# Optimization experiments

Measured on AMD Instinct MI355X. Metric: run time of the kernel, lower is better.

Reference implementation:

```python
import jax, jax.numpy as jnp
import numpy as np

D, N = 4, 2048  # d marginals, n bins


def setup_inputs() -> dict:
    key = jax.random.key(0)
    x = jax.random.uniform(key, (D, N), dtype=jnp.float32)
    return {"x": x}


def reference(x):
    # Greedy multi-marginal EMD (dEMD.forward with computeDual=False).
    # Sequential algorithm: at each step, look at the 'front' value of each of
    # the d rows (AA[i, idx[i]]), take the minimum mass, pay cost
    # (max(idx)-min(idx)) * minval, subtract it from every front, and advance
    # the pointer of the (first) argmin row. Loop ends when any pointer hits n.
    d, n = x.shape
    steps = d * (n - 1) + 1  # exact worst-case iteration count
    rows = jnp.arange(d)

    def step(carry, _):
        AA, idx, obj, done = carry
        vals = AA[rows, idx]                        # (d,) front values
        minval = jnp.min(vals)
        ind = jnp.argmin(vals)                      # first min, like vals.index(min)
        cost = (jnp.max(idx) - jnp.min(idx)).astype(AA.dtype)  # OBJ(idx)
        obj = obj + jnp.where(done, jnp.zeros((), AA.dtype), cost * minval)
        AA_new = AA.at[rows, idx].add(-minval)
        AA = jnp.where(done, AA, AA_new)
        idx_new = jnp.where(done, idx, idx.at[ind].add(1))
        done = done | jnp.any(idx_new >= n)
        return (AA, idx_new, obj, done), None

    init = (x,
            jnp.zeros(d, dtype=jnp.int32),
            jnp.zeros((), dtype=x.dtype),
            jnp.asarray(False))
    (_, _, obj, _), _ = jax.lax.scan(step, init, None, length=steps)
    return obj
```

## Files before the change

kernel.cpp:

```cpp
#include <hip/hip_runtime.h>


constexpr int D       = 4;
constexpr int N       = 2048;
constexpr int THREADS = 256;
constexpr int PER_LANE = N / 64;

__global__ __launch_bounds__(THREADS)
void demd_kernel(const float* __restrict__ x, float* __restrict__ out) {
    __shared__ float  S[D][N];
    __shared__ double red[THREADS];

    const int t    = threadIdx.x;
    const int wave = t >> 6;
    const int lane = t & 63;

    {
        const float* row = x + wave * N + lane * PER_LANE;
        float v[PER_LANE];
        #pragma unroll
        for (int k = 0; k < PER_LANE / 4; ++k) {
            float4 f = ((const float4*)row)[k];
            v[4*k+0] = f.x; v[4*k+1] = f.y; v[4*k+2] = f.z; v[4*k+3] = f.w;
        }
        double tot = 0.0;
        #pragma unroll
        for (int k = 0; k < PER_LANE; ++k) tot += (double)v[k];

        double scan = tot;
        #pragma unroll
        for (int off = 1; off < 64; off <<= 1) {
            double up = __shfl_up(scan, off, 64);
            if (lane >= off) scan += up;
        }
        double run = scan - tot;
        float* Srow = &S[wave][lane * PER_LANE];
        #pragma unroll
        for (int k = 0; k < PER_LANE; ++k) {
            run += (double)v[k];
            Srow[k] = (float)run;
        }
    }
    __syncthreads();

    float tend = S[0][N - 1];
    #pragma unroll
    for (int r = 1; r < D; ++r) tend = fminf(tend, S[r][N - 1]);

    double acc = 0.0;
    #pragma unroll
    for (int k = 0; k < N / THREADS; ++k) {
        const int j = t + k * THREADS;
        float a = S[0][j];
        float b = a;
        #pragma unroll
        for (int r = 1; r < D; ++r) {
            float s = S[r][j];
            a = fminf(a, s);
            b = fmaxf(b, s);
        }
        acc += (double)((tend - a) - fmaxf(0.0f, tend - b));
    }
    red[t] = acc;
    __syncthreads();
    #pragma unroll
    for (int s = THREADS / 2; s > 0; s >>= 1) {
        if (t < s) red[t] += red[t + s];
        __syncthreads();
    }
    if (t == 0) out[0] = (float)red[0];
}

extern "C" void kernel_launch(void* const* d_in, const int* in_sizes, int n_in,
                              void* d_out, int out_size, void* d_ws, size_t ws_size,
                              hipStream_t stream) {
    (void)in_sizes; (void)n_in; (void)d_ws; (void)ws_size; (void)out_size;
    const float* x = (const float*)d_in[0];
    float* out = (float*)d_out;
    demd_kernel<<<1, THREADS, 0, stream>>>(x, out);
}
```

Before: 53.82 us.

## Collapse dEMD kernel to a single wavefront with register-resident prefix sums

Replaces the four-wave block with one 64-lane wavefront. Each lane holds all four rows of its chunk in registers, computes the four prefix scans with shuffles, and evaluates the min/max cost term on the fly without going through shared memory or __syncthreads. The final reduction uses wave shuffles, and accumulation switches from double to float. This removes LDS traffic and barriers, but each lane now does 4x the serial work, register pressure rises, and float accumulation may lose accuracy.

```diff
diff --git a/kernel.cpp b/kernel.cpp
--- a/kernel.cpp
+++ b/kernel.cpp
@@ -1,74 +1,71 @@
 #include <hip/hip_runtime.h>
 
 
-constexpr int D       = 4;
-constexpr int N       = 2048;
-constexpr int THREADS = 256;
+constexpr int D        = 4;
+constexpr int N        = 2048;
 constexpr int PER_LANE = N / 64;
 
-__global__ __launch_bounds__(THREADS)
+__global__ __launch_bounds__(64)
 void demd_kernel(const float* __restrict__ x, float* __restrict__ out) {
-    __shared__ float  S[D][N];
-    __shared__ double red[THREADS];
+    const int lane = threadIdx.x;
 
-    const int t    = threadIdx.x;
-    const int wave = t >> 6;
-    const int lane = t & 63;
-
-    {
-        const float* row = x + wave * N + lane * PER_LANE;
-        float v[PER_LANE];
+    float v[D][PER_LANE];
+    #pragma unroll
+    for (int r = 0; r < D; ++r) {
+        const float4* src = (const float4*)(x + r * N + lane * PER_LANE);
         #pragma unroll
         for (int k = 0; k < PER_LANE / 4; ++k) {
-            float4 f = ((const float4*)row)[k];
-            v[4*k+0] = f.x; v[4*k+1] = f.y; v[4*k+2] = f.z; v[4*k+3] = f.w;
-        }
-        double tot = 0.0;
-        #pragma unroll
-        for (int k = 0; k < PER_LANE; ++k) tot += (double)v[k];
-
-        double scan = tot;
-        #pragma unroll
-        for (int off = 1; off < 64; off <<= 1) {
-            double up = __shfl_up(scan, off, 64);
-            if (lane >= off) scan += up;
-        }
-        double run = scan - tot;
-        float* Srow = &S[wave][lane * PER_LANE];
-        #pragma unroll
-        for (int k = 0; k < PER_LANE; ++k) {
-            run += (double)v[k];
-            Srow[k] = (float)run;
+            float4 f = src[k];
+            v[r][4*k+0] = f.x; v[r][4*k+1] = f.y;
+            v[r][4*k+2] = f.z; v[r][4*k+3] = f.w;
         }
     }
-    __syncthreads();
 
-    float tend = S[0][N - 1];
+    float tot[D];
     #pragma unroll
-    for (int r = 1; r < D; ++r) tend = fminf(tend, S[r][N - 1]);
+    for (int r = 0; r < D; ++r) {
+        float s = 0.0f;
+        #pragma unroll
+        for (int k = 0; k < PER_LANE; ++k) s += v[r][k];
+        tot[r] = s;
+    }
 
-    double acc = 0.0;
+    float scan[D];
     #pragma unroll
-    for (int k = 0; k < N / THREADS; ++k) {
-        const int j = t + k * THREADS;
-        float a = S[0][j];
-        float b = a;
+    for (int r = 0; r < D; ++r) scan[r] = tot[r];
+    #pragma unroll
+    for (int off = 1; off < 64; off <<= 1) {
         #pragma unroll
-        for (int r = 1; r < D; ++r) {
-            float s = S[r][j];
-            a = fminf(a, s);
-            b = fmaxf(b, s);
+        for (int r = 0; r < D; ++r) {
+            float up = __shfl_up(scan[r], off, 64);
+            if (lane >= off) scan[r] += up;
         }
-        acc += (double)((tend - a) - fmaxf(0.0f, tend - b));
     }
-    red[t] = acc;
-    __syncthreads();
+
+    float tend = __shfl(scan[0], 63, 64);
     #pragma unroll
-    for (int s = THREADS / 2; s > 0; s >>= 1) {
-        if (t < s) red[t] += red[t + s];
-        __syncthreads();
+    for (int r = 1; r < D; ++r) tend = fminf(tend, __shfl(scan[r], 63, 64));
+
+    float run[D];
+    #pragma unroll
+    for (int r = 0; r < D; ++r) run[r] = scan[r] - tot[r];
+
+    float acc = 0.0f;
+    #pragma unroll
+    for (int k = 0; k < PER_LANE; ++k) {
+        #pragma unroll
+        for (int r = 0; r < D; ++r) run[r] += v[r][k];
+        float a01 = fminf(run[0], run[1]), a23 = fminf(run[2], run[3]);
+        float b01 = fmaxf(run[0], run[1]), b23 = fmaxf(run[2], run[3]);
+        float a = fminf(a01, a23);
+        float b = fmaxf(b01, b23);
+        acc += (tend - a) - fmaxf(0.0f, tend - b);
     }
-    if (t == 0) out[0] = (float)red[0];
+
+    #pragma unroll
+    for (int off = 32; off > 0; off >>= 1)
+        acc += __shfl_down(acc, off, 64);
+    if (lane == 0) out[0] = acc;
 }
 
 extern "C" void kernel_launch(void* const* d_in, const int* in_sizes, int n_in,
@@ -77,5 +74,5 @@
     (void)in_sizes; (void)n_in; (void)d_ws; (void)ws_size; (void)out_size;
     const float* x = (const float*)d_in[0];
     float* out = (float*)d_out;
-    demd_kernel<<<1, THREADS, 0, stream>>>(x, out);
+    demd_kernel<<<1, 64, 0, stream>>>(x, out);
 }
```

Result: no change. 52.97 us (-1.6%).
